# Kernel tuning notes

Measured on AMD Instinct MI355X. Metric: run time of the kernel, lower is better.

Reference implementation:

```python
import jax, jax.numpy as jnp
import numpy as np


def setup_inputs() -> dict:
    key = jax.random.key(0)
    k1, _ = jax.random.split(key)
    x = jax.random.normal(k1, (2, 16, 16, 16, 64), dtype=jnp.float32)
    gamma = jnp.ones((1,), dtype=jnp.float32)  # learned scalar (zeros at init; ones to make output nontrivial)
    return {"x": x, "gamma": gamma}


def reference(x, gamma):
    # x: (B, D, H, W, C); faithful to the Keras layer: flatten spatial dims,
    # energy = Q @ Q^T over the N=D*H*W axis, softmax(axis=-1), attn @ Q,
    # then gamma-scaled residual add.
    B, D, H, W, C = x.shape
    N = D * H * W
    q = x.reshape(B, N, C)                            # proj_query (B, N, C)
    energy = jnp.einsum('bnc,bmc->bnm', q, q)          # (B, N, N)
    attn = jax.nn.softmax(energy, axis=-1)
    out = jnp.einsum('bnm,bmc->bnc', attn, q)          # (B, N, C)
    out = out.reshape(B, D, H, W, C)
    return gamma * out + x
```

## Files before the change

### kernel.cpp

```cpp
#include <hip/hip_runtime.h>
#include <hip/hip_bf16.h>
#include <math.h>


#define NN 4096
#define CC 64
#define LOG2E 1.4426950408889634f

typedef __attribute__((ext_vector_type(4))) float f32x4;
typedef __attribute__((ext_vector_type(16))) float f32x16;
typedef __attribute__((ext_vector_type(8))) short bf16x8;
typedef __attribute__((ext_vector_type(4))) short bf16x4;
typedef unsigned short u16;
typedef __attribute__((ext_vector_type(4))) u16 u16x4;
typedef __attribute__((ext_vector_type(8))) u16 u16x8;
typedef __attribute__((ext_vector_type(2))) unsigned u32x2;

__device__ inline u16 f2bf(float f) {
  union { float f; unsigned u; } v; v.f = f;
  unsigned r = (v.u + 0x7fffu + ((v.u >> 16) & 1u)) >> 16;
  return (u16)r;
}
__device__ inline float bf2f(short h) {
  union { unsigned u; float f; } v;
  v.u = ((unsigned)(unsigned short)h) << 16;
  return v.f;
}
__device__ inline unsigned fbits(float f) {
  union { float f; unsigned u; } v; v.f = f;
  return v.u;
}
__device__ inline unsigned cvtpk(float lo, float hi) {
  unsigned d;
  asm("v_cvt_pk_bf16_f32 %0, %1, %2" : "=v"(d) : "v"(lo), "v"(hi));
  return d;
}
__device__ inline bf16x8 cvt8(f32x4 a, f32x4 b) {
  bf16x8 r;
  r[0] = (short)f2bf(a[0]); r[1] = (short)f2bf(a[1]);
  r[2] = (short)f2bf(a[2]); r[3] = (short)f2bf(a[3]);
  r[4] = (short)f2bf(b[0]); r[5] = (short)f2bf(b[1]);
  r[6] = (short)f2bf(b[2]); r[7] = (short)f2bf(b[3]);
  return r;
}

__global__ __launch_bounds__(256) void prep_kernel(const float* __restrict__ x,
                                                   u16* __restrict__ Qb,
                                                   u16* __restrict__ Vt) {
  __shared__ u16 t[64][20];
  int b = blockIdx.x >> 8;
  int n0 = (blockIdx.x & 255) << 4;
  const f32x4* x4 = (const f32x4*)(x + ((size_t)b * NN + n0) * CC);
  u16* qb = Qb + ((size_t)b * NN + n0) * CC;
  {
    int idx4 = threadIdx.x;
    int i = idx4 >> 4, cg = idx4 & 15;
    f32x4 v = x4[idx4];
    u16x4 h;
    h[0] = f2bf(v[0]); h[1] = f2bf(v[1]); h[2] = f2bf(v[2]); h[3] = f2bf(v[3]);
    *(u16x4*)(qb + (size_t)i * CC + cg * 4) = h;
    t[cg * 4 + 0][i] = h[0]; t[cg * 4 + 1][i] = h[1];
    t[cg * 4 + 2][i] = h[2]; t[cg * 4 + 3][i] = h[3];
  }
  __syncthreads();
  int kb = n0 >> 6, kw0 = n0 & 63;
  {
    int idx4 = threadIdx.x;
    int c = idx4 >> 2, i4 = (idx4 & 3) * 4;
    u16x4 h = *(const u16x4*)(&t[c][i4]);
    *(u16x4*)(Vt + (((size_t)b * (NN / 64) + kb) * 64 + c) * 64 + kw0 + i4) = h;
  }
}

template <int S>
__global__ __launch_bounds__(512, 4) void attn_split(
    const u16* __restrict__ Qb, const u16* __restrict__ Vt,
    u16* __restrict__ Opart, float* __restrict__ lpart) {
  constexpr int KPS = NN / S;
  constexpr int ITERS = KPS / 64;
  const int lane = threadIdx.x & 63;
  const int w = threadIdx.x >> 6;
  const int wk = w & 1, wr4 = w >> 1;
  const int hf = lane >> 5, l31 = lane & 31, c8 = lane & 7;
  const int blk = blockIdx.x;
  const int b = blk / (32 * S);
  const int rg = (blk / S) & 31;
  const int s = blk % S;

  __shared__ __align__(16) char smem[34816];
  u16* KT = (u16*)smem;
  u16* VT = (u16*)(smem + 16384);

  const u16* Qbase = Qb + (size_t)b * NN * CC;
  const u16* Vbase = Vt + (size_t)b * NN * CC;
  const int row0 = rg * 128 + wr4 * 32;

  bf16x8 qs[4];
  float m_sc;
  {
    const u16* qp = Qbase + (size_t)(row0 + l31) * CC + hf * 8;
    float msum = 0.f;
#pragma unroll
    for (int sl = 0; sl < 4; ++sl) {
      bf16x8 r0 = *(const bf16x8*)(qp + sl * 16);
      bf16x8 t;
#pragma unroll
      for (int j = 0; j < 8; ++j) {
        float a = bf2f(r0[j]);
        u16 hs = f2bf(a * LOG2E);
        t[j] = (short)hs;
        msum += bf2f((short)hs) * a;
      }
      qs[sl] = t;
    }
    msum += __shfl_xor(msum, 32);
    m_sc = msum;
  }

  f32x16 zero16;
#pragma unroll
  for (int r = 0; r < 16; ++r) zero16[r] = 0.f;
  f32x16 acc[2] = {zero16, zero16};
  float l_loc = 0.f;

  const int g8 = lane >> 3;
  const int swz = c8 ^ g8;
  const u16* kptr = Qbase + (size_t)(s * KPS + w * 8 + g8) * CC + swz * 8;
  const u16* vptr = Vbase + (size_t)(s * (KPS >> 6)) * 4096 + (size_t)(w * 8 + g8) * 64 + swz * 8;

#define STAGE(p, it)                                                          \
  {                                                                           \
    __builtin_amdgcn_global_load_lds(                                         \
        (const __attribute__((address_space(1))) unsigned*)(kptr + (size_t)(it) * 4096),       \
        (__attribute__((address_space(3))) unsigned*)&KT[(p) * 4096 + (w * 8) * 64], 16, 0, 0); \
    __builtin_amdgcn_global_load_lds(                                         \
        (const __attribute__((address_space(1))) unsigned*)(vptr + (size_t)(it) * 4096),       \
        (__attribute__((address_space(3))) unsigned*)&VT[(p) * 4096 + (w * 8) * 64], 16, 0, 0); \
  }

  STAGE(0, 0)
  STAGE(1, 1)

#pragma unroll
  for (int i = 0; i < ITERS; ++i) {
    if (i + 1 < ITERS)
      asm volatile("s_waitcnt vmcnt(2)" ::: "memory");
    else
      asm volatile("s_waitcnt vmcnt(0)" ::: "memory");
    __builtin_amdgcn_sched_barrier(0);
    __builtin_amdgcn_s_barrier();
    __builtin_amdgcn_sched_barrier(0);
    const int p = i & 1;
    const u16* KTp = KT + p * 4096;
    const u16* VTp = VT + p * 4096;

    f32x16 sx = zero16;
    __builtin_amdgcn_s_setprio(1);
#pragma unroll
    for (int sl = 0; sl < 4; ++sl) {
      bf16x8 kf = *(const bf16x8*)&KTp[(wk * 32 + l31) * 64 + ((sl * 2 + hf) ^ c8) * 8];
      sx = __builtin_amdgcn_mfma_f32_32x32x16_bf16(kf, qs[sl], sx, 0, 0, 0);
    }
    __builtin_amdgcn_s_setprio(0);

    float p16[16];
#pragma unroll
    for (int r = 0; r < 16; ++r) p16[r] = exp2f(sx[r] - m_sc);
#pragma unroll
    for (int r = 0; r < 16; ++r) l_loc += p16[r];
    unsigned own[4][2], sh[4][2];
#pragma unroll
    for (int q = 0; q < 4; ++q) {
      own[q][0] = cvtpk(p16[4 * q + 0], p16[4 * q + 1]);
      own[q][1] = cvtpk(p16[4 * q + 2], p16[4 * q + 3]);
    }
#pragma unroll
    for (int q = 0; q < 4; ++q) {
      sh[q][0] = (unsigned)__shfl_xor((int)own[q][0], 32);
      sh[q][1] = (unsigned)__shfl_xor((int)own[q][1], 32);
    }
    bf16x8 pf[2];
#pragma unroll
    for (int ks = 0; ks < 2; ++ks) {
      unsigned d0 = hf ? sh[2 * ks + 1][0] : own[2 * ks][0];
      unsigned d1 = hf ? sh[2 * ks + 1][1] : own[2 * ks][1];
      unsigned d2 = hf ? own[2 * ks + 1][0] : sh[2 * ks][0];
      unsigned d3 = hf ? own[2 * ks + 1][1] : sh[2 * ks][1];
      bf16x8 f;
      ((unsigned*)&f)[0] = d0; ((unsigned*)&f)[1] = d1;
      ((unsigned*)&f)[2] = d2; ((unsigned*)&f)[3] = d3;
      pf[ks] = f;
    }

    __builtin_amdgcn_s_setprio(1);
#pragma unroll
    for (int cg = 0; cg < 2; ++cg) {
#pragma unroll
      for (int ks = 0; ks < 2; ++ks) {
        bf16x8 vf = *(const bf16x8*)&VTp[(cg * 32 + l31) * 64 + ((4 * wk + 2 * ks + hf) ^ c8) * 8];
        acc[cg] = __builtin_amdgcn_mfma_f32_32x32x16_bf16(vf, pf[ks], acc[cg], 0, 0, 0);
      }
    }
    __builtin_amdgcn_s_setprio(0);
    __builtin_amdgcn_sched_barrier(0);
    __builtin_amdgcn_s_barrier();
    __builtin_amdgcn_sched_barrier(0);
    if (i + 2 < ITERS) STAGE(p, i + 2)
  }
#undef STAGE

  l_loc += __shfl_xor(l_loc, 32);
  float* LDSO = (float*)smem;
  float* LDSL = (float*)(smem + 64 * 132 * 4);
  const int qcol = wr4 * 32 + l31;
  if (wk == 1) {
#pragma unroll
    for (int cg = 0; cg < 2; ++cg)
#pragma unroll
      for (int r = 0; r < 16; ++r) {
        int ch = cg * 32 + (r & 3) + 8 * (r >> 2) + 4 * hf;
        LDSO[ch * 132 + qcol] = acc[cg][r];
      }
  }
  if (lane < 32) LDSL[wk * 128 + qcol] = l_loc;
  __syncthreads();
  if (wk == 0) {
#pragma unroll
    for (int cg = 0; cg < 2; ++cg)
#pragma unroll
      for (int r = 0; r < 16; ++r) {
        int ch = cg * 32 + (r & 3) + 8 * (r >> 2) + 4 * hf;
        LDSO[ch * 132 + qcol] += acc[cg][r];
      }
  }
  __syncthreads();

  size_t pbase = (((size_t)(b * 32 + rg)) * S + s) * (128 * 64);
  size_t lbase = (((size_t)(b * 32 + rg)) * S + s) * 128;
  {
    int row = threadIdx.x >> 2;
    int cq = threadIdx.x & 3;
    u16x8 o0, o1;
#pragma unroll
    for (int j = 0; j < 8; ++j) {
      o0[j] = f2bf(LDSO[(cq * 16 + j) * 132 + row]);
      o1[j] = f2bf(LDSO[(cq * 16 + 8 + j) * 132 + row]);
    }
    *(u16x8*)(Opart + pbase + (size_t)row * 64 + cq * 16) = o0;
    *(u16x8*)(Opart + pbase + (size_t)row * 64 + cq * 16 + 8) = o1;
  }
  if (threadIdx.x < 128)
    lpart[lbase + threadIdx.x] = LDSL[threadIdx.x] + LDSL[128 + threadIdx.x];
}

template <int S>
__global__ __launch_bounds__(256) void epi_kernel(
    const float* __restrict__ x, const float* __restrict__ gamma,
    const u16* __restrict__ Opart, const float* __restrict__ lpart,
    float* __restrict__ out) {
  int t = blockIdx.x * 256 + threadIdx.x;
  int cg = t & 15;
  int n = (t >> 4) & (NN - 1);
  int b = t >> 16;
  int rb = n >> 7, lr = n & 127;
  size_t obase = ((size_t)(b * 32 + rb) * S) * 8192 + (size_t)lr * 64 + cg * 4;
  size_t lbase = ((size_t)(b * 32 + rb) * S) * 128 + lr;
  f32x4 sO = {0.f, 0.f, 0.f, 0.f};
  float sL = 0.f;
#pragma unroll
  for (int s = 0; s < S; ++s) {
    u16x4 o4 = *(const u16x4*)(Opart + obase + (size_t)s * 8192);
    sL += lpart[lbase + (size_t)s * 128];
    sO[0] += bf2f((short)o4[0]); sO[1] += bf2f((short)o4[1]);
    sO[2] += bf2f((short)o4[2]); sO[3] += bf2f((short)o4[3]);
  }
  size_t xi = (((size_t)b * NN + n) * CC + cg * 4);
  f32x4 xv = *(const f32x4*)(x + xi);
  float g = gamma[0], inv = 1.f / sL;
  f32x4 ov;
#pragma unroll
  for (int j = 0; j < 4; ++j) ov[j] = g * (sO[j] * inv) + xv[j];
  *(f32x4*)(((float*)out) + xi) = ov;
}

template <int WPB>
__global__ __launch_bounds__(WPB * 64, 4) void attn_fast(
    const float* __restrict__ x, const float* __restrict__ gamma,
    const u16* __restrict__ Qb, const u16* __restrict__ Vt,
    float* __restrict__ out) {
  const int w = threadIdx.x >> 6;
  const int lane = threadIdx.x & 63;
  const int quad = lane >> 4, col = lane & 15;
  const int b = blockIdx.x >> 8;
  const int tile = (blockIdx.x & 255) << 4;

  extern __shared__ char smem[];
  float* Osh = (float*)smem;
  float* lsh = Osh + WPB * 1024;
  u16* pl = (u16*)(lsh + WPB * 16) + w * 2176;

  const size_t xoff = (size_t)b * NN * CC;
  const u16* Qbase = Qb + xoff;
  const u16* Vbase = Vt + xoff;

  bf16x8 qf0 = *(const bf16x8*)(Qbase + (size_t)(tile + col) * CC + quad * 8);
  bf16x8 qf1 = *(const bf16x8*)(Qbase + (size_t)(tile + col) * CC + 32 + quad * 8);

  float msum = 0.f;
#pragma unroll
  for (int j = 0; j < 8; ++j) {
    float a = bf2f(qf0[j]), c = bf2f(qf1[j]);
    msum += a * a + c * c;
  }
  msum += __shfl_xor(msum, 16);
  msum += __shfl_xor(msum, 32);
  float m_i[4];
#pragma unroll
  for (int r = 0; r < 4; ++r) m_i[r] = __shfl(msum, quad * 4 + r);

  f32x4 zero = {0.f, 0.f, 0.f, 0.f};
  f32x4 acc[4] = {zero, zero, zero, zero};
  float l_i[4] = {0.f, 0.f, 0.f, 0.f};

  const int k0 = w * (NN / WPB);
#pragma unroll 2
  for (int kt = k0; kt < k0 + NN / WPB; kt += 64) {
    u16* plc = pl + ((kt >> 6) & 1) * 1088;
    f32x4 sx[4];
#pragma unroll
    for (int t = 0; t < 4; ++t) {
      const u16* kp = Qbase + (size_t)(kt + t * 16 + col) * CC + quad * 8;
      bf16x8 ka = *(const bf16x8*)kp;
      bf16x8 kb = *(const bf16x8*)(kp + 32);
      sx[t] = __builtin_amdgcn_mfma_f32_16x16x32_bf16(qf0, ka, zero, 0, 0, 0);
      sx[t] = __builtin_amdgcn_mfma_f32_16x16x32_bf16(qf1, kb, sx[t], 0, 0, 0);
    }
#pragma unroll
    for (int t = 0; t < 4; ++t) {
#pragma unroll
      for (int r = 0; r < 4; ++r) {
        float p = __expf(sx[t][r] - m_i[r]);
        l_i[r] += p;
        plc[(quad * 4 + r) * 68 + t * 16 + col] = f2bf(p);
      }
    }
    bf16x8 pf0 = *(const bf16x8*)(plc + col * 68 + quad * 8);
    bf16x8 pf1 = *(const bf16x8*)(plc + col * 68 + 32 + quad * 8);
#pragma unroll
    for (int cg = 0; cg < 4; ++cg) {
      const u16* vp = Vbase + (((size_t)(kt >> 6)) * 64 + cg * 16 + col) * 64 + quad * 8;
      bf16x8 v0 = *(const bf16x8*)vp;
      bf16x8 v1 = *(const bf16x8*)(vp + 32);
      acc[cg] = __builtin_amdgcn_mfma_f32_16x16x32_bf16(pf0, v0, acc[cg], 0, 0, 0);
      acc[cg] = __builtin_amdgcn_mfma_f32_16x16x32_bf16(pf1, v1, acc[cg], 0, 0, 0);
    }
  }

#pragma unroll
  for (int r = 0; r < 4; ++r)
#pragma unroll
    for (int off = 1; off < 16; off <<= 1) l_i[r] += __shfl_xor(l_i[r], off, 16);
#pragma unroll
  for (int r = 0; r < 4; ++r) {
    int row = quad * 4 + r;
    Osh[(w * 16 + row) * 64 + col]      = acc[0][r];
    Osh[(w * 16 + row) * 64 + col + 16] = acc[1][r];
    Osh[(w * 16 + row) * 64 + col + 32] = acc[2][r];
    Osh[(w * 16 + row) * 64 + col + 48] = acc[3][r];
    if (col == 0) lsh[w * 16 + row] = l_i[r];
  }
  __syncthreads();

  float g = gamma[0];
  for (int row = w; row < 16; row += WPB) {
    float L = 0.f, val = 0.f;
#pragma unroll
    for (int w2 = 0; w2 < WPB; ++w2) {
      L += lsh[w2 * 16 + row];
      val += Osh[(w2 * 16 + row) * 64 + lane];
    }
    size_t o = xoff + (size_t)(tile + row) * CC + lane;
    out[o] = g * (val / L) + x[o];
  }
}

template <int WPB>
__global__ __launch_bounds__(512) void attn_fb(const float* __restrict__ x,
                                               const float* __restrict__ gamma,
                                               float* __restrict__ out) {
  const int w = threadIdx.x >> 6;
  const int lane = threadIdx.x & 63;
  const int quad = lane >> 4, col = lane & 15;
  const int b = blockIdx.x >> 8;
  const int tile = (blockIdx.x & 255) << 4;

  extern __shared__ char smem[];
  float* Osh = (float*)smem;
  float* msh = Osh + WPB * 1024;
  float* lsh = msh + WPB * 16;
  u16* pl = (u16*)(lsh + WPB * 16) + w * 768;
  u16* vt = (u16*)(lsh + WPB * 16) + WPB * 768 + w * 2176;

  const size_t xoff = (size_t)b * NN * CC;
  const f32x4* x4 = (const f32x4*)(x + xoff);

  bf16x8 qf0, qf1;
  {
    int ri = (tile + col) * 16 + quad * 2;
    qf0 = cvt8(x4[ri], x4[ri + 1]);
    qf1 = cvt8(x4[ri + 8], x4[ri + 9]);
  }
  f32x4 zero = {0.f, 0.f, 0.f, 0.f};
  f32x4 acc0 = zero, acc1 = zero, acc2 = zero, acc3 = zero;
  float m_i[4], l_i[4];
#pragma unroll
  for (int r = 0; r < 4; ++r) { m_i[r] = -1e30f; l_i[r] = 0.f; }

  const int k0 = w * (NN / WPB);
  for (int kt = k0; kt < k0 + NN / WPB; kt += 32) {
    bf16x8 k00, k01, k10, k11;
    {
      int kb = (kt + col) * 16 + quad * 2;
      k00 = cvt8(x4[kb], x4[kb + 1]);
      k01 = cvt8(x4[kb + 8], x4[kb + 9]);
      k10 = cvt8(x4[kb + 256], x4[kb + 257]);
      k11 = cvt8(x4[kb + 264], x4[kb + 265]);
#pragma unroll
      for (int h = 0; h < 2; ++h) {
        bf16x8 va = h ? k10 : k00, vb = h ? k11 : k01;
        int base = (h * 16 + col) * 68 + quad * 8;
        *(bf16x4*)(vt + base) = __builtin_shufflevector(va, va, 0, 1, 2, 3);
        *(bf16x4*)(vt + base + 4) = __builtin_shufflevector(va, va, 4, 5, 6, 7);
        *(bf16x4*)(vt + base + 32) = __builtin_shufflevector(vb, vb, 0, 1, 2, 3);
        *(bf16x4*)(vt + base + 36) = __builtin_shufflevector(vb, vb, 4, 5, 6, 7);
      }
    }
    f32x4 s0 = zero, s1 = zero;
    s0 = __builtin_amdgcn_mfma_f32_16x16x32_bf16(qf0, k00, s0, 0, 0, 0);
    s0 = __builtin_amdgcn_mfma_f32_16x16x32_bf16(qf1, k01, s0, 0, 0, 0);
    s1 = __builtin_amdgcn_mfma_f32_16x16x32_bf16(qf0, k10, s1, 0, 0, 0);
    s1 = __builtin_amdgcn_mfma_f32_16x16x32_bf16(qf1, k11, s1, 0, 0, 0);

    float p0[4], p1[4], alpha[4];
#pragma unroll
    for (int r = 0; r < 4; ++r) {
      float mx = fmaxf(s0[r], s1[r]);
#pragma unroll
      for (int off = 1; off < 16; off <<= 1) mx = fmaxf(mx, __shfl_xor(mx, off, 16));
      float mn = fmaxf(m_i[r], mx);
      alpha[r] = __expf(m_i[r] - mn);
      p0[r] = __expf(s0[r] - mn);
      p1[r] = __expf(s1[r] - mn);
      float rs = p0[r] + p1[r];
#pragma unroll
      for (int off = 1; off < 16; off <<= 1) rs += __shfl_xor(rs, off, 16);
      l_i[r] = l_i[r] * alpha[r] + rs;
      m_i[r] = mn;
    }
#pragma unroll
    for (int r = 0; r < 4; ++r) {
      acc0[r] *= alpha[r]; acc1[r] *= alpha[r];
      acc2[r] *= alpha[r]; acc3[r] *= alpha[r];
    }
#pragma unroll
    for (int r = 0; r < 4; ++r) {
      pl[(quad * 4 + r) * 24 + col] = f2bf(p0[r]);
      pl[384 + (quad * 4 + r) * 24 + col] = f2bf(p1[r]);
    }
    bf16x8 pf = *(const bf16x8*)(pl + (quad >> 1) * 384 + col * 24 + (quad & 1) * 8);

    bf16x8 v0, v1, v2, v3;
#pragma unroll
    for (int j = 0; j < 8; ++j) {
      int rb = (quad * 8 + j) * 68 + col;
      v0[j] = (short)vt[rb];
      v1[j] = (short)vt[rb + 16];
      v2[j] = (short)vt[rb + 32];
      v3[j] = (short)vt[rb + 48];
    }
    acc0 = __builtin_amdgcn_mfma_f32_16x16x32_bf16(pf, v0, acc0, 0, 0, 0);
    acc1 = __builtin_amdgcn_mfma_f32_16x16x32_bf16(pf, v1, acc1, 0, 0, 0);
    acc2 = __builtin_amdgcn_mfma_f32_16x16x32_bf16(pf, v2, acc2, 0, 0, 0);
    acc3 = __builtin_amdgcn_mfma_f32_16x16x32_bf16(pf, v3, acc3, 0, 0, 0);
  }

#pragma unroll
  for (int r = 0; r < 4; ++r) {
    int row = quad * 4 + r;
    Osh[(w * 16 + row) * 64 + col] = acc0[r];
    Osh[(w * 16 + row) * 64 + col + 16] = acc1[r];
    Osh[(w * 16 + row) * 64 + col + 32] = acc2[r];
    Osh[(w * 16 + row) * 64 + col + 48] = acc3[r];
    if (col == 0) { msh[w * 16 + row] = m_i[r]; lsh[w * 16 + row] = l_i[r]; }
  }
  __syncthreads();

  float g = gamma[0];
  for (int row = w; row < 16; row += WPB) {
    float M = -1e30f;
#pragma unroll
    for (int w2 = 0; w2 < WPB; ++w2) M = fmaxf(M, msh[w2 * 16 + row]);
    float L = 0.f, val = 0.f;
#pragma unroll
    for (int w2 = 0; w2 < WPB; ++w2) {
      float e = __expf(msh[w2 * 16 + row] - M);
      L += lsh[w2 * 16 + row] * e;
      val += Osh[(w2 * 16 + row) * 64 + lane] * e;
    }
    size_t o = xoff + (size_t)(tile + row) * CC + lane;
    out[o] = g * (val / L) + x[o];
  }
}

extern "C" void kernel_launch(void* const* d_in, const int* in_sizes, int n_in,
                              void* d_out, int out_size, void* d_ws, size_t ws_size,
                              hipStream_t stream) {
  const float* x = (const float*)d_in[0];
  const float* gamma = (const float*)d_in[1];
  float* out = (float*)d_out;

  constexpr int S = 8;
  constexpr size_t kQV = (size_t)2 * 2 * NN * CC * sizeof(u16);
  constexpr size_t kOp = (size_t)2 * 32 * S * 128 * 64 * sizeof(u16);
  constexpr size_t kLp = (size_t)2 * 32 * S * 128 * sizeof(float);
  if (ws_size >= kQV + kOp + kLp) {
    u16* Qb = (u16*)d_ws;
    u16* Vt = Qb + (size_t)2 * NN * CC;
    u16* Opart = (u16*)((char*)d_ws + kQV);
    float* lpart = (float*)((char*)d_ws + kQV + kOp);
    prep_kernel<<<512, 256, 0, stream>>>(x, Qb, Vt);
    attn_split<S><<<2 * 32 * S, 512, 0, stream>>>(Qb, Vt, Opart, lpart);
    epi_kernel<S><<<(2 * NN * 16) / 256, 256, 0, stream>>>(x, gamma, Opart, lpart, out);
  } else if (ws_size >= kQV) {
    u16* Qb = (u16*)d_ws;
    u16* Vt = Qb + (size_t)2 * NN * CC;
    prep_kernel<<<512, 256, 0, stream>>>(x, Qb, Vt);
    constexpr int SM = 8 * 1024 * 4 + 8 * 16 * 4 + 8 * 2176 * 2;
    attn_fast<8><<<512, 512, SM, stream>>>(x, gamma, Qb, Vt, out);
  } else {
    constexpr int SM4 = 4 * (1024 + 32) * 4 + 4 * 768 * 2 + 4 * 2176 * 2;
    attn_fb<4><<<512, 256, SM4, stream>>>(x, gamma, out);
  }
}
```

Measured before the change: 82.57 us.

## Fuse bf16 prep into split attention kernel, converting fp32 tiles to LDS in-loop

Result: slower. 91.60 us (+10.9%).

```diff
diff --git a/kernel.cpp b/kernel.cpp
--- a/kernel.cpp
+++ b/kernel.cpp
@@ -14,7 +14,6 @@
 typedef unsigned short u16;
 typedef __attribute__((ext_vector_type(4))) u16 u16x4;
 typedef __attribute__((ext_vector_type(8))) u16 u16x8;
-typedef __attribute__((ext_vector_type(2))) unsigned u32x2;
 
 __device__ inline u16 f2bf(float f) {
   union { float f; unsigned u; } v; v.f = f;
@@ -25,10 +24,6 @@
   union { unsigned u; float f; } v;
   v.u = ((unsigned)(unsigned short)h) << 16;
   return v.f;
-}
-__device__ inline unsigned fbits(float f) {
-  union { float f; unsigned u; } v; v.f = f;
-  return v.u;
 }
 __device__ inline unsigned cvtpk(float lo, float hi) {
   unsigned d;
@@ -44,37 +39,9 @@
   return r;
 }
 
-__global__ __launch_bounds__(256) void prep_kernel(const float* __restrict__ x,
-                                                   u16* __restrict__ Qb,
-                                                   u16* __restrict__ Vt) {
-  __shared__ u16 t[64][20];
-  int b = blockIdx.x >> 8;
-  int n0 = (blockIdx.x & 255) << 4;
-  const f32x4* x4 = (const f32x4*)(x + ((size_t)b * NN + n0) * CC);
-  u16* qb = Qb + ((size_t)b * NN + n0) * CC;
-  {
-    int idx4 = threadIdx.x;
-    int i = idx4 >> 4, cg = idx4 & 15;
-    f32x4 v = x4[idx4];
-    u16x4 h;
-    h[0] = f2bf(v[0]); h[1] = f2bf(v[1]); h[2] = f2bf(v[2]); h[3] = f2bf(v[3]);
-    *(u16x4*)(qb + (size_t)i * CC + cg * 4) = h;
-    t[cg * 4 + 0][i] = h[0]; t[cg * 4 + 1][i] = h[1];
-    t[cg * 4 + 2][i] = h[2]; t[cg * 4 + 3][i] = h[3];
-  }
-  __syncthreads();
-  int kb = n0 >> 6, kw0 = n0 & 63;
-  {
-    int idx4 = threadIdx.x;
-    int c = idx4 >> 2, i4 = (idx4 & 3) * 4;
-    u16x4 h = *(const u16x4*)(&t[c][i4]);
-    *(u16x4*)(Vt + (((size_t)b * (NN / 64) + kb) * 64 + c) * 64 + kw0 + i4) = h;
-  }
-}
-
 template <int S>
 __global__ __launch_bounds__(512, 4) void attn_split(
-    const u16* __restrict__ Qb, const u16* __restrict__ Vt,
+    const float* __restrict__ x,
     u16* __restrict__ Opart, float* __restrict__ lpart) {
   constexpr int KPS = NN / S;
   constexpr int ITERS = KPS / 64;
@@ -87,29 +54,27 @@
   const int rg = (blk / S) & 31;
   const int s = blk % S;
 
-  __shared__ __align__(16) char smem[34816];
+  __shared__ __align__(16) char smem[36864];
   u16* KT = (u16*)smem;
   u16* VT = (u16*)(smem + 16384);
 
-  const u16* Qbase = Qb + (size_t)b * NN * CC;
-  const u16* Vbase = Vt + (size_t)b * NN * CC;
+  const float* xb = x + (size_t)b * NN * CC;
   const int row0 = rg * 128 + wr4 * 32;
 
   bf16x8 qs[4];
   float m_sc;
   {
-    const u16* qp = Qbase + (size_t)(row0 + l31) * CC + hf * 8;
+    const float* qp = xb + (size_t)(row0 + l31) * CC;
     float msum = 0.f;
 #pragma unroll
     for (int sl = 0; sl < 4; ++sl) {
-      bf16x8 r0 = *(const bf16x8*)(qp + sl * 16);
       bf16x8 t;
 #pragma unroll
       for (int j = 0; j < 8; ++j) {
-        float a = bf2f(r0[j]);
+        float a = qp[sl * 16 + hf * 8 + j];
         u16 hs = f2bf(a * LOG2E);
         t[j] = (short)hs;
-        msum += bf2f((short)hs) * a;
+        msum += bf2f((short)hs) * bf2f((short)f2bf(a));
       }
       qs[sl] = t;
     }
@@ -123,42 +88,47 @@
   f32x16 acc[2] = {zero16, zero16};
   float l_loc = 0.f;
 
-  const int g8 = lane >> 3;
-  const int swz = c8 ^ g8;
-  const u16* kptr = Qbase + (size_t)(s * KPS + w * 8 + g8) * CC + swz * 8;
-  const u16* vptr = Vbase + (size_t)(s * (KPS >> 6)) * 4096 + (size_t)(w * 8 + g8) * 64 + swz * 8;
-
-#define STAGE(p, it)                                                          \
-  {                                                                           \
-    __builtin_amdgcn_global_load_lds(                                         \
-        (const __attribute__((address_space(1))) unsigned*)(kptr + (size_t)(it) * 4096),       \
-        (__attribute__((address_space(3))) unsigned*)&KT[(p) * 4096 + (w * 8) * 64], 16, 0, 0); \
-    __builtin_amdgcn_global_load_lds(                                         \
-        (const __attribute__((address_space(1))) unsigned*)(vptr + (size_t)(it) * 4096),       \
-        (__attribute__((address_space(3))) unsigned*)&VT[(p) * 4096 + (w * 8) * 64], 16, 0, 0); \
-  }
-
-  STAGE(0, 0)
-  STAGE(1, 1)
+  const int lk = w * 8 + (lane >> 3);
+  const int chsw = c8 ^ (lk & 7);
+  const float* ksrc = xb + (size_t)(s * KPS + lk) * CC + chsw * 8;
+
+  f32x4 ra, rb;
+
+#define LOADT(it)                                                            \
+  {                                                                          \
+    const f32x4* p4 = (const f32x4*)(ksrc + (size_t)(it) * 64 * CC);         \
+    ra = p4[0]; rb = p4[1];                                                  \
+  }
+#define WRITET(p)                                                            \
+  {                                                                          \
+    bf16x8 kv;                                                               \
+    ((unsigned*)&kv)[0] = cvtpk(ra[0], ra[1]);                               \
+    ((unsigned*)&kv)[1] = cvtpk(ra[2], ra[3]);                               \
+    ((unsigned*)&kv)[2] = cvtpk(rb[0], rb[1]);                               \
+    ((unsigned*)&kv)[3] = cvtpk(rb[2], rb[3]);                               \
+    *(bf16x8*)&KT[(p) * 4096 + lk * 64 + c8 * 8] = kv;                       \
+    u16* vcol = &VT[(p) * 4224 + lk];                                        \
+    _Pragma("unroll")                                                        \
+    for (int j = 0; j < 8; ++j) vcol[(chsw * 8 + j) * 66] = (u16)kv[j];      \
+  }
+
+  LOADT(0)
+  WRITET(0)
+  if (ITERS > 1) LOADT(1)
+  __syncthreads();
 
 #pragma unroll
   for (int i = 0; i < ITERS; ++i) {
-    if (i + 1 < ITERS)
-      asm volatile("s_waitcnt vmcnt(2)" ::: "memory");
-    else
-      asm volatile("s_waitcnt vmcnt(0)" ::: "memory");
-    __builtin_amdgcn_sched_barrier(0);
-    __builtin_amdgcn_s_barrier();
-    __builtin_amdgcn_sched_barrier(0);
     const int p = i & 1;
-    const u16* KTp = KT + p * 4096;
-    const u16* VTp = VT + p * 4096;
+    if (i + 1 < ITERS) WRITET(p ^ 1)
+    if (i + 2 < ITERS) LOADT(i + 2)
 
     f32x16 sx = zero16;
     __builtin_amdgcn_s_setprio(1);
 #pragma unroll
     for (int sl = 0; sl < 4; ++sl) {
-      bf16x8 kf = *(const bf16x8*)&KTp[(wk * 32 + l31) * 64 + ((sl * 2 + hf) ^ c8) * 8];
+      bf16x8 kf = *(const bf16x8*)&KT[p * 4096 + (wk * 32 + l31) * 64 +
+                                      ((sl * 2 + hf) ^ (l31 & 7)) * 8];
       sx = __builtin_amdgcn_mfma_f32_32x32x16_bf16(kf, qs[sl], sx, 0, 0, 0);
     }
     __builtin_amdgcn_s_setprio(0);
@@ -197,17 +167,16 @@
     for (int cg = 0; cg < 2; ++cg) {
 #pragma unroll
       for (int ks = 0; ks < 2; ++ks) {
-        bf16x8 vf = *(const bf16x8*)&VTp[(cg * 32 + l31) * 64 + ((4 * wk + 2 * ks + hf) ^ c8) * 8];
+        bf16x8 vf = *(const bf16x8*)&VT[p * 4224 + (cg * 32 + l31) * 66 +
+                                        (4 * wk + 2 * ks + hf) * 8];
         acc[cg] = __builtin_amdgcn_mfma_f32_32x32x16_bf16(vf, pf[ks], acc[cg], 0, 0, 0);
       }
     }
     __builtin_amdgcn_s_setprio(0);
-    __builtin_amdgcn_sched_barrier(0);
-    __builtin_amdgcn_s_barrier();
-    __builtin_amdgcn_sched_barrier(0);
-    if (i + 2 < ITERS) STAGE(p, i + 2)
-  }
-#undef STAGE
+    __syncthreads();
+  }
+#undef LOADT
+#undef WRITET
 
   l_loc += __shfl_xor(l_loc, 32);
   float* LDSO = (float*)smem;
@@ -284,107 +253,6 @@
 }
 
 template <int WPB>
-__global__ __launch_bounds__(WPB * 64, 4) void attn_fast(
-    const float* __restrict__ x, const float* __restrict__ gamma,
-    const u16* __restrict__ Qb, const u16* __restrict__ Vt,
-    float* __restrict__ out) {
-  const int w = threadIdx.x >> 6;
-  const int lane = threadIdx.x & 63;
-  const int quad = lane >> 4, col = lane & 15;
-  const int b = blockIdx.x >> 8;
-  const int tile = (blockIdx.x & 255) << 4;
-
-  extern __shared__ char smem[];
-  float* Osh = (float*)smem;
-  float* lsh = Osh + WPB * 1024;
-  u16* pl = (u16*)(lsh + WPB * 16) + w * 2176;
-
-  const size_t xoff = (size_t)b * NN * CC;
-  const u16* Qbase = Qb + xoff;
-  const u16* Vbase = Vt + xoff;
-
-  bf16x8 qf0 = *(const bf16x8*)(Qbase + (size_t)(tile + col) * CC + quad * 8);
-  bf16x8 qf1 = *(const bf16x8*)(Qbase + (size_t)(tile + col) * CC + 32 + quad * 8);
-
-  float msum = 0.f;
-#pragma unroll
-  for (int j = 0; j < 8; ++j) {
-    float a = bf2f(qf0[j]), c = bf2f(qf1[j]);
-    msum += a * a + c * c;
-  }
-  msum += __shfl_xor(msum, 16);
-  msum += __shfl_xor(msum, 32);
-  float m_i[4];
-#pragma unroll
-  for (int r = 0; r < 4; ++r) m_i[r] = __shfl(msum, quad * 4 + r);
-
-  f32x4 zero = {0.f, 0.f, 0.f, 0.f};
-  f32x4 acc[4] = {zero, zero, zero, zero};
-  float l_i[4] = {0.f, 0.f, 0.f, 0.f};
-
-  const int k0 = w * (NN / WPB);
-#pragma unroll 2
-  for (int kt = k0; kt < k0 + NN / WPB; kt += 64) {
-    u16* plc = pl + ((kt >> 6) & 1) * 1088;
-    f32x4 sx[4];
-#pragma unroll
-    for (int t = 0; t < 4; ++t) {
-      const u16* kp = Qbase + (size_t)(kt + t * 16 + col) * CC + quad * 8;
-      bf16x8 ka = *(const bf16x8*)kp;
-      bf16x8 kb = *(const bf16x8*)(kp + 32);
-      sx[t] = __builtin_amdgcn_mfma_f32_16x16x32_bf16(qf0, ka, zero, 0, 0, 0);
-      sx[t] = __builtin_amdgcn_mfma_f32_16x16x32_bf16(qf1, kb, sx[t], 0, 0, 0);
-    }
-#pragma unroll
-    for (int t = 0; t < 4; ++t) {
-#pragma unroll
-      for (int r = 0; r < 4; ++r) {
-        float p = __expf(sx[t][r] - m_i[r]);
-        l_i[r] += p;
-        plc[(quad * 4 + r) * 68 + t * 16 + col] = f2bf(p);
-      }
-    }
-    bf16x8 pf0 = *(const bf16x8*)(plc + col * 68 + quad * 8);
-    bf16x8 pf1 = *(const bf16x8*)(plc + col * 68 + 32 + quad * 8);
-#pragma unroll
-    for (int cg = 0; cg < 4; ++cg) {
-      const u16* vp = Vbase + (((size_t)(kt >> 6)) * 64 + cg * 16 + col) * 64 + quad * 8;
-      bf16x8 v0 = *(const bf16x8*)vp;
-      bf16x8 v1 = *(const bf16x8*)(vp + 32);
-      acc[cg] = __builtin_amdgcn_mfma_f32_16x16x32_bf16(pf0, v0, acc[cg], 0, 0, 0);
-      acc[cg] = __builtin_amdgcn_mfma_f32_16x16x32_bf16(pf1, v1, acc[cg], 0, 0, 0);
-    }
-  }
-
-#pragma unroll
-  for (int r = 0; r < 4; ++r)
-#pragma unroll
-    for (int off = 1; off < 16; off <<= 1) l_i[r] += __shfl_xor(l_i[r], off, 16);
-#pragma unroll
-  for (int r = 0; r < 4; ++r) {
-    int row = quad * 4 + r;
-    Osh[(w * 16 + row) * 64 + col]      = acc[0][r];
-    Osh[(w * 16 + row) * 64 + col + 16] = acc[1][r];
-    Osh[(w * 16 + row) * 64 + col + 32] = acc[2][r];
-    Osh[(w * 16 + row) * 64 + col + 48] = acc[3][r];
-    if (col == 0) lsh[w * 16 + row] = l_i[r];
-  }
-  __syncthreads();
-
-  float g = gamma[0];
-  for (int row = w; row < 16; row += WPB) {
-    float L = 0.f, val = 0.f;
-#pragma unroll
-    for (int w2 = 0; w2 < WPB; ++w2) {
-      L += lsh[w2 * 16 + row];
-      val += Osh[(w2 * 16 + row) * 64 + lane];
-    }
-    size_t o = xoff + (size_t)(tile + row) * CC + lane;
-    out[o] = g * (val / L) + x[o];
-  }
-}
-
-template <int WPB>
 __global__ __launch_bounds__(512) void attn_fb(const float* __restrict__ x,
                                                const float* __restrict__ gamma,
                                                float* __restrict__ out) {
@@ -520,23 +388,13 @@
   float* out = (float*)d_out;
 
   constexpr int S = 8;
-  constexpr size_t kQV = (size_t)2 * 2 * NN * CC * sizeof(u16);
   constexpr size_t kOp = (size_t)2 * 32 * S * 128 * 64 * sizeof(u16);
   constexpr size_t kLp = (size_t)2 * 32 * S * 128 * sizeof(float);
-  if (ws_size >= kQV + kOp + kLp) {
-    u16* Qb = (u16*)d_ws;
-    u16* Vt = Qb + (size_t)2 * NN * CC;
-    u16* Opart = (u16*)((char*)d_ws + kQV);
-    float* lpart = (float*)((char*)d_ws + kQV + kOp);
-    prep_kernel<<<512, 256, 0, stream>>>(x, Qb, Vt);
-    attn_split<S><<<2 * 32 * S, 512, 0, stream>>>(Qb, Vt, Opart, lpart);
+  if (ws_size >= kOp + kLp) {
+    u16* Opart = (u16*)d_ws;
+    float* lpart = (float*)((char*)d_ws + kOp);
+    attn_split<S><<<2 * 32 * S, 512, 0, stream>>>(x, Opart, lpart);
     epi_kernel<S><<<(2 * NN * 16) / 256, 256, 0, stream>>>(x, gamma, Opart, lpart, out);
-  } else if (ws_size >= kQV) {
-    u16* Qb = (u16*)d_ws;
-    u16* Vt = Qb + (size_t)2 * NN * CC;
-    prep_kernel<<<512, 256, 0, stream>>>(x, Qb, Vt);
-    constexpr int SM = 8 * 1024 * 4 + 8 * 16 * 4 + 8 * 2176 * 2;
-    attn_fast<8><<<512, 512, SM, stream>>>(x, gamma, Qb, Vt, out);
   } else {
     constexpr int SM4 = 4 * (1024 + 32) * 4 + 4 * 768 * 2 + 4 * 2176 * 2;
     attn_fb<4><<<512, 256, SM4, stream>>>(x, gamma, out);
```
